# Optimization experiments

Hardware: AMD Instinct MI355X
Metric: run time of the kernel (lower is better)

## Reference

```python
import jax, jax.numpy as jnp
import numpy as np

N_NODES = 100000
N_EDGES = 1600000
D_IN = 64
D_OUT = 64
EDGE_DIM = 1


def setup_inputs() -> dict:
    key = jax.random.key(0)
    ks = jax.random.split(key, 6)
    x = jax.random.normal(ks[0], (N_NODES, D_IN), dtype=jnp.float32)
    edge_index = jax.random.randint(ks[1], (2, N_EDGES), 0, N_NODES, dtype=jnp.int64)
    edge_attr = jax.random.uniform(ks[2], (N_EDGES, EDGE_DIM), dtype=jnp.float32)
    # xavier-uniform-ish weight
    limit = float(np.sqrt(6.0 / (D_IN + D_OUT)))
    weight = jax.random.uniform(ks[3], (D_IN, D_OUT), minval=-limit, maxval=limit, dtype=jnp.float32)
    lim2 = float(np.sqrt(1.0 / EDGE_DIM))
    ew_W = jax.random.uniform(ks[4], (EDGE_DIM, D_OUT), minval=-lim2, maxval=lim2, dtype=jnp.float32)
    ew_b = jnp.zeros((D_OUT,), dtype=jnp.float32)
    bias = jnp.zeros((D_OUT,), dtype=jnp.float32)
    return {"x": x, "edge_index": edge_index, "edge_attr": edge_attr,
            "weight": weight, "ew_W": ew_W, "ew_b": ew_b, "bias": bias}


def reference(x, edge_index, edge_attr, weight, ew_W, ew_b, bias):
    n_nodes = x.shape[0]
    src = edge_index[0]  # i: message source
    dst = edge_index[1]  # j: message destination
    x_t = x @ weight                                   # [N, D_OUT]
    edge_w = jax.nn.sigmoid(edge_attr @ ew_W + ew_b)   # [E, D_OUT]
    msg = x_t[src] * edge_w                            # [E, D_OUT] gather-multiply
    out = jax.ops.segment_sum(msg, dst, num_segments=n_nodes)  # scatter-add
    return out + bias
```

## Files before the change

kernel.cpp:

```cpp
#include <hip/hip_runtime.h>
#include <hip/hip_bf16.h>
#include <math.h>

#define D 64
#define SCAN_B 256

typedef __hip_bfloat16 bf16;
typedef __attribute__((ext_vector_type(8))) short bf16x8;
typedef __attribute__((ext_vector_type(4))) float f32x4;

static __device__ __forceinline__ short f2bf(float f) {
    unsigned u = __float_as_uint(f);
    u = (u + 0x7FFFu + ((u >> 16) & 1u)) >> 16;
    return (short)u;
}

static __device__ __forceinline__ float fsig(float a, float nwd, float nbd) {
    float e = __expf(fmaf(a, nwd, nbd));
    return __builtin_amdgcn_rcpf(1.f + e);
}

__global__ __launch_bounds__(256) void hist_kernel(const int* __restrict__ ei,
                                                   int* __restrict__ counts,
                                                   int* __restrict__ rank,
                                                   int n_edges) {
    const int gid = blockIdx.x * blockDim.x + threadIdx.x;
    const int nth = gridDim.x * blockDim.x;
    for (int e = gid; e < n_edges; e += nth) {
        int dst = ei[n_edges + e];
        rank[e] = atomicAdd(&counts[dst], 1);
    }
}

__global__ __launch_bounds__(256) void gemm_mfma_kernel(const float* __restrict__ x,
                                                        const float* __restrict__ W,
                                                        bf16* __restrict__ xt,
                                                        int n_nodes) {
    __shared__ float Ws[64 * 64];
    {
        const float4* src = reinterpret_cast<const float4*>(W);
        float4* dstp = reinterpret_cast<float4*>(Ws);
        for (int i = threadIdx.x; i < 1024; i += 256) dstp[i] = src[i];
    }
    __syncthreads();

    const int lane  = threadIdx.x & 63;
    const int wv    = threadIdx.x >> 6;
    const int m0    = blockIdx.x * 64 + wv * 16;
    const int half  = lane >> 4;
    const int idx16 = lane & 15;
    const int k0    = half * 8;

    bf16x8 bfrag[4][2];
#pragma unroll
    for (int t = 0; t < 4; ++t) {
#pragma unroll
        for (int h = 0; h < 2; ++h) {
            bf16x8 f;
#pragma unroll
            for (int j = 0; j < 8; ++j)
                f[j] = f2bf(Ws[(h * 32 + k0 + j) * 64 + t * 16 + idx16]);
            bfrag[t][h] = f;
        }
    }

    const int am = m0 + idx16;
    const bool valid = (am < n_nodes);
    const float* arow = x + (size_t)(valid ? am : 0) * 64;

    f32x4 acc[4] = {{0.f, 0.f, 0.f, 0.f}, {0.f, 0.f, 0.f, 0.f},
                    {0.f, 0.f, 0.f, 0.f}, {0.f, 0.f, 0.f, 0.f}};

#pragma unroll
    for (int h = 0; h < 2; ++h) {
        bf16x8 afrag = {0, 0, 0, 0, 0, 0, 0, 0};
        if (valid) {
            float4 p0 = *reinterpret_cast<const float4*>(arow + h * 32 + k0);
            float4 p1 = *reinterpret_cast<const float4*>(arow + h * 32 + k0 + 4);
            afrag[0] = f2bf(p0.x); afrag[1] = f2bf(p0.y);
            afrag[2] = f2bf(p0.z); afrag[3] = f2bf(p0.w);
            afrag[4] = f2bf(p1.x); afrag[5] = f2bf(p1.y);
            afrag[6] = f2bf(p1.z); afrag[7] = f2bf(p1.w);
        }
#pragma unroll
        for (int t = 0; t < 4; ++t)
            acc[t] = __builtin_amdgcn_mfma_f32_16x16x32_bf16(afrag, bfrag[t][h],
                                                             acc[t], 0, 0, 0);
    }

    const int srow0 = m0 + half * 4;
#pragma unroll
    for (int r = 0; r < 4; ++r) {
        int row = srow0 + r;
        if (row < n_nodes) {
#pragma unroll
            for (int t = 0; t < 4; ++t)
                xt[(size_t)row * 64 + t * 16 + idx16] = __float2bfloat16(acc[t][r]);
        }
    }
}

__global__ __launch_bounds__(SCAN_B) void scan1_kernel(const int* __restrict__ c,
                                                       int* __restrict__ excl,
                                                       int* __restrict__ partials,
                                                       int n) {
    __shared__ int s[SCAN_B];
    int i = blockIdx.x * SCAN_B + threadIdx.x;
    int v = (i < n) ? c[i] : 0;
    s[threadIdx.x] = v;
    __syncthreads();
    for (int off = 1; off < SCAN_B; off <<= 1) {
        int t = (threadIdx.x >= off) ? s[threadIdx.x - off] : 0;
        __syncthreads();
        s[threadIdx.x] += t;
        __syncthreads();
    }
    if (i < n) excl[i] = s[threadIdx.x] - v;
    if (threadIdx.x == SCAN_B - 1) partials[blockIdx.x] = s[SCAN_B - 1];
}

__global__ __launch_bounds__(SCAN_B) void scan23_kernel(int* __restrict__ offsets,
                                                        const int* __restrict__ partials,
                                                        int n, int n_edges) {
    __shared__ int red[SCAN_B];
    int psum = 0;
    for (int i = threadIdx.x; i < blockIdx.x; i += SCAN_B) psum += partials[i];
    red[threadIdx.x] = psum;
    __syncthreads();
    for (int off = SCAN_B / 2; off > 0; off >>= 1) {
        if (threadIdx.x < off) red[threadIdx.x] += red[threadIdx.x + off];
        __syncthreads();
    }
    int base = red[0];
    int i = blockIdx.x * SCAN_B + threadIdx.x;
    if (i < n) offsets[i] += base;
    if (blockIdx.x == 0 && threadIdx.x == 0) offsets[n] = n_edges;
}

__global__ __launch_bounds__(256) void fill_kernel(const int* __restrict__ ei,
                                                   const float* __restrict__ ea,
                                                   const int* __restrict__ offs,
                                                   const int* __restrict__ rank,
                                                   int2* __restrict__ csr,
                                                   int n_edges) {
    int e = blockIdx.x * blockDim.x + threadIdx.x;
    if (e >= n_edges) return;
    int dst = ei[n_edges + e];
    int pos = offs[dst] + rank[e];
    long long v = ((long long)__float_as_int(ea[e]) << 32) | (unsigned)ei[e];
    __builtin_nontemporal_store(v, (long long*)(csr + pos));
}

__global__ __launch_bounds__(256) void gather_kernel(const int* __restrict__ offsets,
                                                     const int2* __restrict__ csr,
                                                     const bf16* __restrict__ xt,
                                                     const float* __restrict__ ewW,
                                                     const float* __restrict__ ewb,
                                                     const float* __restrict__ bias,
                                                     float* __restrict__ out,
                                                     int n_nodes) {
    const int d = threadIdx.x & 63;
    const int node = (blockIdx.x * blockDim.x + threadIdx.x) >> 6;
    if (node >= n_nodes) return;

    const float nwd = -ewW[d];
    const float nbd = -ewb[d];
    const int start = offsets[node];
    const int end = offsets[node + 1];

    float acc = 0.f;
    int k = start;
    for (; k + 8 <= end; k += 8) {
        long long q[8];
        float xv[8];
#pragma unroll
        for (int j = 0; j < 8; ++j)
            q[j] = __builtin_nontemporal_load((const long long*)(csr + k + j));
#pragma unroll
        for (int j = 0; j < 8; ++j) {
            unsigned off = ((unsigned)(int)(unsigned)q[j] << 6) + d;
            xv[j] = __bfloat162float(xt[off]);
        }
#pragma unroll
        for (int j = 0; j < 8; ++j) {
            float a = __int_as_float((int)(q[j] >> 32));
            acc = fmaf(xv[j], fsig(a, nwd, nbd), acc);
        }
    }
    for (; k + 4 <= end; k += 4) {
        long long q0 = __builtin_nontemporal_load((const long long*)(csr + k + 0));
        long long q1 = __builtin_nontemporal_load((const long long*)(csr + k + 1));
        long long q2 = __builtin_nontemporal_load((const long long*)(csr + k + 2));
        long long q3 = __builtin_nontemporal_load((const long long*)(csr + k + 3));
        float x0 = __bfloat162float(xt[(((unsigned)(int)(unsigned)q0) << 6) + d]);
        float x1 = __bfloat162float(xt[(((unsigned)(int)(unsigned)q1) << 6) + d]);
        float x2 = __bfloat162float(xt[(((unsigned)(int)(unsigned)q2) << 6) + d]);
        float x3 = __bfloat162float(xt[(((unsigned)(int)(unsigned)q3) << 6) + d]);
        acc = fmaf(x0, fsig(__int_as_float((int)(q0 >> 32)), nwd, nbd), acc);
        acc = fmaf(x1, fsig(__int_as_float((int)(q1 >> 32)), nwd, nbd), acc);
        acc = fmaf(x2, fsig(__int_as_float((int)(q2 >> 32)), nwd, nbd), acc);
        acc = fmaf(x3, fsig(__int_as_float((int)(q3 >> 32)), nwd, nbd), acc);
    }
    for (; k < end; ++k) {
        long long q = __builtin_nontemporal_load((const long long*)(csr + k));
        float xv = __bfloat162float(xt[(((unsigned)(int)(unsigned)q) << 6) + d]);
        acc = fmaf(xv, fsig(__int_as_float((int)(q >> 32)), nwd, nbd), acc);
    }
    float r = acc + bias[d];
    __builtin_nontemporal_store(r, out + (size_t)node * 64 + d);
}

__global__ __launch_bounds__(256) void init_out_kernel(float* __restrict__ out,
                                                       const float* __restrict__ bias,
                                                       int n_f4) {
    int i = blockIdx.x * blockDim.x + threadIdx.x;
    if (i >= n_f4) return;
    float4 b4 = reinterpret_cast<const float4*>(bias)[i & 15];
    reinterpret_cast<float4*>(out)[i] = b4;
}

__global__ __launch_bounds__(256) void edge_atomic_kernel(const int* __restrict__ ei,
                                                          const float* __restrict__ ea,
                                                          const bf16* __restrict__ xt,
                                                          const float* __restrict__ ewW,
                                                          const float* __restrict__ ewb,
                                                          float* __restrict__ out,
                                                          int n_edges) {
    const int gid = blockIdx.x * blockDim.x + threadIdx.x;
    const int d0 = (gid & 15) * 4;
    int e = gid >> 4;
    const int estride = (gridDim.x * blockDim.x) >> 4;
    for (; e < n_edges; e += estride) {
        const int src = ei[e];
        const int dst = ei[n_edges + e];
        const float a = ea[e];
        float xv0 = __bfloat162float(xt[(size_t)src * 64 + d0 + 0]);
        float xv1 = __bfloat162float(xt[(size_t)src * 64 + d0 + 1]);
        float xv2 = __bfloat162float(xt[(size_t)src * 64 + d0 + 2]);
        float xv3 = __bfloat162float(xt[(size_t)src * 64 + d0 + 3]);
        float w0 = fsig(a, -ewW[d0 + 0], -ewb[d0 + 0]);
        float w1 = fsig(a, -ewW[d0 + 1], -ewb[d0 + 1]);
        float w2 = fsig(a, -ewW[d0 + 2], -ewb[d0 + 2]);
        float w3 = fsig(a, -ewW[d0 + 3], -ewb[d0 + 3]);
        float* op = out + (size_t)dst * 64 + d0;
        unsafeAtomicAdd(op + 0, xv0 * w0);
        unsafeAtomicAdd(op + 1, xv1 * w1);
        unsafeAtomicAdd(op + 2, xv2 * w2);
        unsafeAtomicAdd(op + 3, xv3 * w3);
    }
}

extern "C" void kernel_launch(void* const* d_in, const int* in_sizes, int n_in,
                              void* d_out, int out_size, void* d_ws, size_t ws_size,
                              hipStream_t stream) {
    const float* x      = (const float*)d_in[0];
    const int*   ei     = (const int*)d_in[1];
    const float* ea     = (const float*)d_in[2];
    const float* weight = (const float*)d_in[3];
    const float* ewW    = (const float*)d_in[4];
    const float* ewb    = (const float*)d_in[5];
    const float* bias   = (const float*)d_in[6];
    float* out = (float*)d_out;

    const int n_nodes = in_sizes[0] / D;
    const int n_edges = in_sizes[2];

    char* ws = (char*)d_ws;
    const size_t xt_bytes   = (size_t)n_nodes * D * sizeof(bf16);
    const size_t off_off    = (xt_bytes + 7) & ~(size_t)7;
    const size_t off_bytes  = ((size_t)n_nodes + 4) * sizeof(int);
    const size_t part_off   = off_off + off_bytes;
    const size_t part_bytes = 512 * sizeof(int);
    const size_t rank_off   = part_off + part_bytes;
    const size_t rank_bytes = (size_t)n_edges * sizeof(int);
    size_t csr_off          = (rank_off + rank_bytes + 7) & ~(size_t)7;
    const size_t csr_bytes  = (size_t)n_edges * sizeof(int2);
    const size_t need       = csr_off + csr_bytes;

    bf16* xt   = (bf16*)(ws);
    int*  offs = (int*)(ws + off_off);
    int*  parts= (int*)(ws + part_off);
    int*  rank = (int*)(ws + rank_off);
    int2* csr  = (int2*)(ws + csr_off);

    const bool have_ws = (ws_size >= need);
    const int gemm_grid = (n_nodes + 63) / 64;

    if (have_ws) {
        hipMemsetAsync(offs, 0, off_bytes, stream);
        hist_kernel<<<2048, 256, 0, stream>>>(ei, offs, rank, n_edges);
        gemm_mfma_kernel<<<gemm_grid, 256, 0, stream>>>(x, weight, xt, n_nodes);

        const int nscan_blocks = (n_nodes + SCAN_B - 1) / SCAN_B;
        scan1_kernel<<<nscan_blocks, SCAN_B, 0, stream>>>(offs, offs, parts, n_nodes);
        scan23_kernel<<<nscan_blocks, SCAN_B, 0, stream>>>(offs, parts, n_nodes, n_edges);
        fill_kernel<<<(n_edges + 255) / 256, 256, 0, stream>>>(ei, ea, offs, rank, csr, n_edges);
        gather_kernel<<<(n_nodes * 64 + 255) / 256, 256, 0, stream>>>(offs, csr, xt, ewW, ewb,
                                                                      bias, out, n_nodes);
    } else {
        gemm_mfma_kernel<<<gemm_grid, 256, 0, stream>>>(x, weight, xt, n_nodes);
        int n_f4 = n_nodes * (D / 4);
        init_out_kernel<<<(n_f4 + 255) / 256, 256, 0, stream>>>(out, bias, n_f4);
        edge_atomic_kernel<<<4096, 256, 0, stream>>>(ei, ea, xt, ewW, ewb, out, n_edges);
    }
}
```

Measured before the change: 214.1 us.

## Fuse histogram into GEMM kernel and gather two nodes per wave

```diff
diff --git a/kernel.cpp b/kernel.cpp
--- a/kernel.cpp
+++ b/kernel.cpp
@@ -8,40 +8,43 @@
 typedef __hip_bfloat16 bf16;
 typedef __attribute__((ext_vector_type(8))) short bf16x8;
 typedef __attribute__((ext_vector_type(4))) float f32x4;
+typedef __attribute__((ext_vector_type(2))) float f32x2;
 
 static __device__ __forceinline__ short f2bf(float f) {
     unsigned u = __float_as_uint(f);
     u = (u + 0x7FFFu + ((u >> 16) & 1u)) >> 16;
     return (short)u;
 }
-
+static __device__ __forceinline__ float bf2f(unsigned short h) {
+    return __uint_as_float(((unsigned)h) << 16);
+}
 static __device__ __forceinline__ float fsig(float a, float nwd, float nbd) {
     float e = __expf(fmaf(a, nwd, nbd));
     return __builtin_amdgcn_rcpf(1.f + e);
 }
 
-__global__ __launch_bounds__(256) void hist_kernel(const int* __restrict__ ei,
-                                                   int* __restrict__ counts,
-                                                   int* __restrict__ rank,
-                                                   int n_edges) {
-    const int gid = blockIdx.x * blockDim.x + threadIdx.x;
-    const int nth = gridDim.x * blockDim.x;
-    for (int e = gid; e < n_edges; e += nth) {
-        int dst = ei[n_edges + e];
-        rank[e] = atomicAdd(&counts[dst], 1);
-    }
-}
-
-__global__ __launch_bounds__(256) void gemm_mfma_kernel(const float* __restrict__ x,
+__global__ __launch_bounds__(256) void gemm_hist_kernel(const float* __restrict__ x,
                                                         const float* __restrict__ W,
+                                                        const int* __restrict__ ei,
                                                         bf16* __restrict__ xt,
-                                                        int n_nodes) {
+                                                        int* __restrict__ counts,
+                                                        int* __restrict__ rank,
+                                                        int n_nodes, int n_edges) {
     __shared__ float Ws[64 * 64];
     {
         const float4* src = reinterpret_cast<const float4*>(W);
         float4* dstp = reinterpret_cast<float4*>(Ws);
         for (int i = threadIdx.x; i < 1024; i += 256) dstp[i] = src[i];
     }
+
+    const int gid = blockIdx.x * blockDim.x + threadIdx.x;
+    const int nth = gridDim.x * blockDim.x;
+
+    for (int e = gid; e < n_edges; e += nth) {
+        int dst = ei[n_edges + e];
+        rank[e] = atomicAdd(&counts[dst], 1);
+    }
+
     __syncthreads();
 
     const int lane  = threadIdx.x & 63;
@@ -159,55 +162,72 @@
                                                      const float* __restrict__ bias,
                                                      float* __restrict__ out,
                                                      int n_nodes) {
-    const int d = threadIdx.x & 63;
-    const int node = (blockIdx.x * blockDim.x + threadIdx.x) >> 6;
+    const int lane  = threadIdx.x & 63;
+    const int halfw = lane >> 5;
+    const int l     = lane & 31;
+    const int d0    = l * 2;
+    const int wavei = (blockIdx.x * blockDim.x + threadIdx.x) >> 6;
+    const int node  = wavei * 2 + halfw;
     if (node >= n_nodes) return;
 
-    const float nwd = -ewW[d];
-    const float nbd = -ewb[d];
+    const float2 wv = *reinterpret_cast<const float2*>(ewW + d0);
+    const float2 bv = *reinterpret_cast<const float2*>(ewb + d0);
+    const float nw0 = -wv.x, nb0 = -bv.x;
+    const float nw1 = -wv.y, nb1 = -bv.y;
+
     const int start = offsets[node];
-    const int end = offsets[node + 1];
-
-    float acc = 0.f;
+    const int end   = offsets[node + 1];
+
+    float acc0 = 0.f, acc1 = 0.f;
     int k = start;
     for (; k + 8 <= end; k += 8) {
         long long q[8];
-        float xv[8];
+        ushort2 rv[8];
 #pragma unroll
         for (int j = 0; j < 8; ++j)
             q[j] = __builtin_nontemporal_load((const long long*)(csr + k + j));
 #pragma unroll
         for (int j = 0; j < 8; ++j) {
-            unsigned off = ((unsigned)(int)(unsigned)q[j] << 6) + d;
-            xv[j] = __bfloat162float(xt[off]);
+            unsigned off = (((unsigned)(int)(unsigned)q[j]) << 6) + d0;
+            rv[j] = *reinterpret_cast<const ushort2*>(xt + off);
         }
 #pragma unroll
         for (int j = 0; j < 8; ++j) {
             float a = __int_as_float((int)(q[j] >> 32));
-            acc = fmaf(xv[j], fsig(a, nwd, nbd), acc);
+            acc0 = fmaf(bf2f(rv[j].x), fsig(a, nw0, nb0), acc0);
+            acc1 = fmaf(bf2f(rv[j].y), fsig(a, nw1, nb1), acc1);
         }
     }
     for (; k + 4 <= end; k += 4) {
-        long long q0 = __builtin_nontemporal_load((const long long*)(csr + k + 0));
-        long long q1 = __builtin_nontemporal_load((const long long*)(csr + k + 1));
-        long long q2 = __builtin_nontemporal_load((const long long*)(csr + k + 2));
-        long long q3 = __builtin_nontemporal_load((const long long*)(csr + k + 3));
-        float x0 = __bfloat162float(xt[(((unsigned)(int)(unsigned)q0) << 6) + d]);
-        float x1 = __bfloat162float(xt[(((unsigned)(int)(unsigned)q1) << 6) + d]);
-        float x2 = __bfloat162float(xt[(((unsigned)(int)(unsigned)q2) << 6) + d]);
-        float x3 = __bfloat162float(xt[(((unsigned)(int)(unsigned)q3) << 6) + d]);
-        acc = fmaf(x0, fsig(__int_as_float((int)(q0 >> 32)), nwd, nbd), acc);
-        acc = fmaf(x1, fsig(__int_as_float((int)(q1 >> 32)), nwd, nbd), acc);
-        acc = fmaf(x2, fsig(__int_as_float((int)(q2 >> 32)), nwd, nbd), acc);
-        acc = fmaf(x3, fsig(__int_as_float((int)(q3 >> 32)), nwd, nbd), acc);
+        long long q[4];
+        ushort2 rv[4];
+#pragma unroll
+        for (int j = 0; j < 4; ++j)
+            q[j] = __builtin_nontemporal_load((const long long*)(csr + k + j));
+#pragma unroll
+        for (int j = 0; j < 4; ++j) {
+            unsigned off = (((unsigned)(int)(unsigned)q[j]) << 6) + d0;
+            rv[j] = *reinterpret_cast<const ushort2*>(xt + off);
+        }
+#pragma unroll
+        for (int j = 0; j < 4; ++j) {
+            float a = __int_as_float((int)(q[j] >> 32));
+            acc0 = fmaf(bf2f(rv[j].x), fsig(a, nw0, nb0), acc0);
+            acc1 = fmaf(bf2f(rv[j].y), fsig(a, nw1, nb1), acc1);
+        }
     }
     for (; k < end; ++k) {
         long long q = __builtin_nontemporal_load((const long long*)(csr + k));
-        float xv = __bfloat162float(xt[(((unsigned)(int)(unsigned)q) << 6) + d]);
-        acc = fmaf(xv, fsig(__int_as_float((int)(q >> 32)), nwd, nbd), acc);
-    }
-    float r = acc + bias[d];
-    __builtin_nontemporal_store(r, out + (size_t)node * 64 + d);
+        unsigned off = (((unsigned)(int)(unsigned)q) << 6) + d0;
+        ushort2 rv = *reinterpret_cast<const ushort2*>(xt + off);
+        float a = __int_as_float((int)(q >> 32));
+        acc0 = fmaf(bf2f(rv.x), fsig(a, nw0, nb0), acc0);
+        acc1 = fmaf(bf2f(rv.y), fsig(a, nw1, nb1), acc1);
+    }
+    f32x2 o;
+    o.x = acc0 + bias[d0];
+    o.y = acc1 + bias[d0 + 1];
+    __builtin_nontemporal_store(o, reinterpret_cast<f32x2*>(out + (size_t)node * 64 + d0));
 }
 
 __global__ __launch_bounds__(256) void init_out_kernel(float* __restrict__ out,
@@ -287,18 +307,22 @@
     const int gemm_grid = (n_nodes + 63) / 64;
 
     if (have_ws) {
-        hipMemsetAsync(offs, 0, off_bytes, stream);
-        hist_kernel<<<2048, 256, 0, stream>>>(ei, offs, rank, n_edges);
-        gemm_mfma_kernel<<<gemm_grid, 256, 0, stream>>>(x, weight, xt, n_nodes);
+        (void)hipMemsetAsync(offs, 0, off_bytes, stream);
+        gemm_hist_kernel<<<gemm_grid, 256, 0, stream>>>(x, weight, ei, xt, offs, rank,
+                                                        n_nodes, n_edges);
 
         const int nscan_blocks = (n_nodes + SCAN_B - 1) / SCAN_B;
         scan1_kernel<<<nscan_blocks, SCAN_B, 0, stream>>>(offs, offs, parts, n_nodes);
         scan23_kernel<<<nscan_blocks, SCAN_B, 0, stream>>>(offs, parts, n_nodes, n_edges);
         fill_kernel<<<(n_edges + 255) / 256, 256, 0, stream>>>(ei, ea, offs, rank, csr, n_edges);
-        gather_kernel<<<(n_nodes * 64 + 255) / 256, 256, 0, stream>>>(offs, csr, xt, ewW, ewb,
-                                                                      bias, out, n_nodes);
+
+        const int n_waves = (n_nodes + 1) / 2;
+        const int gth = n_waves * 64;
+        gather_kernel<<<(gth + 255) / 256, 256, 0, stream>>>(offs, csr, xt, ewW, ewb,
+                                                             bias, out, n_nodes);
     } else {
-        gemm_mfma_kernel<<<gemm_grid, 256, 0, stream>>>(x, weight, xt, n_nodes);
+        gemm_hist_kernel<<<gemm_grid, 256, 0, stream>>>(x, weight, ei, xt,
+                                                        nullptr, nullptr, n_nodes, 0);
         int n_f4 = n_nodes * (D / 4);
         init_out_kernel<<<(n_f4 + 255) / 256, 256, 0, stream>>>(out, bias, n_f4);
         edge_atomic_kernel<<<4096, 256, 0, stream>>>(ei, ea, xt, ewW, ewb, out, n_edges);
```

Result: faster. 189.8 us (-11.4%).
